# Performance work log

Hardware: AMD Instinct MI355X
Metric: run time of the kernel (lower is better)

Reference implementation:

```python
import jax, jax.numpy as jnp
import numpy as np

EPS = 1e-5  # BatchNorm eps


def _conv3x3(x, w, b):
    # x: [B,C,H,W], w: [O,C,3,3], b: [O]
    y = jax.lax.conv_general_dilated(
        x, w, window_strides=(1, 1), padding=((1, 1), (1, 1)),
        dimension_numbers=("NCHW", "OIHW", "NCHW"))
    return y + b[None, :, None, None]


def _bilinear_gather(x, py, px):
    """Bilinear sample x at fractional coords (zero outside bounds).
    x: [B,C,H,W]; py, px: [B,K,H,W] -> returns [B,C,K,H,W]."""
    B, C, H, W = x.shape
    K = py.shape[1]
    x_flat = x.reshape(B, C, H * W)
    y0 = jnp.floor(py)
    x0 = jnp.floor(px)
    wy1 = py - y0
    wx1 = px - x0
    wy0 = 1.0 - wy1
    wx0 = 1.0 - wx1

    def gather(yi, xi):
        valid = (yi >= 0) & (yi <= H - 1) & (xi >= 0) & (xi <= W - 1)
        yc = jnp.clip(yi, 0, H - 1).astype(jnp.int32)
        xc = jnp.clip(xi, 0, W - 1).astype(jnp.int32)
        idx = (yc * W + xc).reshape(B, 1, K * H * W)
        g = jnp.take_along_axis(x_flat, idx, axis=2).reshape(B, C, K, H, W)
        return g * valid.astype(x.dtype)[:, None]

    val = (gather(y0, x0) * (wy0 * wx0)[:, None]
           + gather(y0, x0 + 1.0) * (wy0 * wx1)[:, None]
           + gather(y0 + 1.0, x0) * (wy1 * wx0)[:, None]
           + gather(y0 + 1.0, x0 + 1.0) * (wy1 * wx1)[:, None])
    return val


def _deform_conv_bn_relu(x, w_off, b_off, w_dcn, b_dcn, gamma, beta):
    B, Ci, H, W = x.shape
    Co = w_dcn.shape[0]
    # offset/mask branch: 27 = 9 dy | 9 dx (cat, then interpreted interleaved) | 9 mask
    om = _conv3x3(x, w_off, b_off)                       # [B,27,H,W]
    offset = jnp.concatenate([om[:, :9], om[:, 9:18]], axis=1)  # [B,18,H,W]
    mask = jax.nn.sigmoid(om[:, 18:27])                  # [B,9,H,W]
    dy = offset[:, 0::2]                                 # [B,9,H,W]
    dx = offset[:, 1::2]                                 # [B,9,H,W]
    # base sampling grid: stride 1, pad 1, dilation 1, 3x3 kernel
    ky = jnp.repeat(jnp.arange(3, dtype=x.dtype), 3)     # [9]
    kx = jnp.tile(jnp.arange(3, dtype=x.dtype), 3)       # [9]
    hh = jnp.arange(H, dtype=x.dtype)
    ww = jnp.arange(W, dtype=x.dtype)
    py = dy + (hh - 1.0)[None, None, :, None] + ky[None, :, None, None]
    px = dx + (ww - 1.0)[None, None, None, :] + kx[None, :, None, None]
    sampled = _bilinear_gather(x, py, px)                # [B,Ci,9,H,W]
    sampled = sampled * mask[:, None]                    # modulated (DCNv2)
    out = jnp.einsum('bckhw,ock->bohw', sampled, w_dcn.reshape(Co, Ci, 9))
    out = out + b_dcn[None, :, None, None]
    # BatchNorm2d (training mode: batch statistics, biased variance) + ReLU
    mean = jnp.mean(out, axis=(0, 2, 3), keepdims=True)
    var = jnp.mean(jnp.square(out - mean), axis=(0, 2, 3), keepdims=True)
    bn = (out - mean) * jax.lax.rsqrt(var + EPS)
    bn = bn * gamma[None, :, None, None] + beta[None, :, None, None]
    return jax.nn.relu(bn)


def setup_inputs() -> dict:
    key = jax.random.key(0)
    k0, k1, k2 = jax.random.split(key, 3)
    B, Ci, Co, H, W = 2, 256, 256, 96, 96
    x = jax.random.normal(k0, (B, Ci, H, W), jnp.float32)
    # small offset-conv weights -> offsets within a few pixels (realistic after training)
    w_off = jax.random.normal(k1, (27, Ci, 3, 3), jnp.float32) * 0.01
    b_off = jnp.zeros((27,), jnp.float32)
    w_dcn = jax.random.normal(k2, (Co, Ci, 3, 3), jnp.float32) * (1.0 / np.sqrt(Ci * 9))
    b_dcn = jnp.zeros((Co,), jnp.float32)
    gamma = jnp.ones((Co,), jnp.float32)
    beta = jnp.zeros((Co,), jnp.float32)
    return {"x": x, "w_off": w_off, "b_off": b_off, "w_dcn": w_dcn,
            "b_dcn": b_dcn, "gamma": gamma, "beta": beta}


def reference(x, w_off, b_off, w_dcn, b_dcn, gamma, beta):
    return _deform_conv_bn_relu(x, w_off, b_off, w_dcn, b_dcn, gamma, beta)
```

## Files before the change

### kernel.cpp

```cpp
#include <hip/hip_runtime.h>


typedef unsigned short ushort_t;
typedef unsigned int uint_t;
typedef __attribute__((ext_vector_type(8))) short bf16x8;
typedef __attribute__((ext_vector_type(4))) float f32x4;
typedef __attribute__((ext_vector_type(2))) float f32x2v;

#define HH 96
#define WW 96
#define HWSZ 9216
#define CI 256
#define CO 256
#define NB 2
#define NPIX 18432
#define KTOT 2304

__device__ __forceinline__ uint_t f2bf(float f) {
  unsigned int u = __float_as_uint(f);
  u += 0x7fffu + ((u >> 16) & 1u);
  return u >> 16;
}
__device__ __forceinline__ float u2f(uint_t u) { return __uint_as_float(u); }
__device__ __forceinline__ float bflo(uint_t u) { return __uint_as_float(u << 16); }
__device__ __forceinline__ float bfhi(uint_t u) { return __uint_as_float(u & 0xffff0000u); }

__device__ __forceinline__ void gload16(const void* g, void* l) {
  __builtin_amdgcn_global_load_lds(
      (const __attribute__((address_space(1))) unsigned int*)g,
      (__attribute__((address_space(3))) unsigned int*)l, 16, 0, 0);
}

__global__ void cvt_w9(const float* __restrict__ w, ushort_t* __restrict__ o) {
  int i = blockIdx.x * 256 + threadIdx.x;
  int oo = i / KTOT;
  int kk = i - oo * KTOT;
  o[(kk >> 3) * 2048 + oo * 8 + (kk & 7)] = (ushort_t)f2bf(w[i]);
}

__global__ void cvt_woff9(const float* __restrict__ w, ushort_t* __restrict__ o) {
  int i = blockIdx.x * 256 + threadIdx.x;
  int m = i / KTOT;
  int kk = i - m * KTOT;
  float v = (m < 27) ? w[m * KTOT + kk] : 0.f;
  o[(kk >> 3) * 256 + m * 8 + (kk & 7)] = (ushort_t)f2bf(v);
}

__global__ __launch_bounds__(512, 2) void off_gemm(
    const float* __restrict__ x, const ushort_t* __restrict__ w27r,
    float* __restrict__ om_part) {
  __shared__ __align__(16) ushort_t A27[2][2048];
  __shared__ __align__(16) ushort_t B64[4096];
  __shared__ uint2 tbl[9][64];

  const int tid = threadIdx.x;
  const int lane = tid & 63, wid = tid >> 6;
  const int p0 = blockIdx.x * 64;
  const int part = blockIdx.y;
  const int bimg = p0 / HWSZ;
  const int hw0 = p0 - bimg * HWSZ;
  const float* xb = x + (size_t)bimg * CI * HWSZ;

  for (int e = tid; e < 576; e += 512) {
    int k = e >> 6, px = e & 63;
    int hw = hw0 + px, h = hw / WW, w_ = hw - h * WW;
    int dy = k / 3 - 1, dx = k % 3 - 1;
    bool ok = (h + dy >= 0) && (h + dy < HH) && (w_ + dx >= 0) && (w_ + dx < WW);
    tbl[k][px] = make_uint2(ok ? (uint_t)(hw + dy * WW + dx) : 0u,
                            ok ? 0x3f800000u : 0u);
  }

  const int lg = lane >> 4, lm = lane & 15;
  const int wr = wid >> 2, wc = wid & 3;
  f32x4 acc = (f32x4){0.f, 0.f, 0.f, 0.f};

  int cj[8], kj[8];
#pragma unroll
  for (int j = 0; j < 8; ++j) {
    int kk = part * 1152 + wid * 8 + j;
    cj[j] = kk / 9;
    kj[j] = kk - 9 * cj[j];
  }
  __syncthreads();

  float rv0[8], rm0[8], rv1[8], rm1[8];
  const int k0 = part * 18;

#define OG_RAW(RV, RM)                                                        \
  { _Pragma("unroll") for (int j = 0; j < 8; ++j) {                           \
      uint2 e_ = tbl[kj[j]][lane];                                            \
      RV[j] = xb[cj[j] * HWSZ + (int)e_.x];                                   \
      RM[j] = u2f(e_.y);                                                      \
      kj[j] += 1; cj[j] += 7;                                                 \
      if (kj[j] == 9) { kj[j] = 0; cj[j] += 1; } } }
#define OG_GA(CH, BUF)                                                        \
  gload16(w27r + (size_t)(CH) * 2048 + (tid & 255) * 8, &A27[BUF][(wid & 3) * 512]);
#define OG_STEP(CUR, RVC, RMC, RVN, RMN, KO)                                  \
  {                                                                           \
    if ((KO) < 17) {                                                          \
      OG_RAW(RVN, RMN)                                                        \
      OG_GA(k0 + (KO) + 1, (CUR) ^ 1)                                         \
      asm volatile("s_waitcnt vmcnt(10)" ::: "memory");                       \
    } else {                                                                  \
      asm volatile("s_waitcnt vmcnt(1)" ::: "memory");                        \
    }                                                                         \
    __builtin_amdgcn_sched_barrier(0);                                        \
    {                                                                         \
      ushort_t sv_[8] __attribute__((aligned(16)));                           \
      _Pragma("unroll") for (int j = 0; j < 8; ++j)                           \
        sv_[j] = (ushort_t)f2bf(RVC[j] * RMC[j]);                             \
      *(uint4*)&B64[tid * 8] = *(const uint4*)sv_;                            \
    }                                                                         \
    if ((KO) < 17) asm volatile("s_waitcnt vmcnt(9) lgkmcnt(0)" ::: "memory"); \
    else           asm volatile("s_waitcnt vmcnt(0) lgkmcnt(0)" ::: "memory"); \
    __builtin_amdgcn_s_barrier();                                             \
    __builtin_amdgcn_sched_barrier(0);                                        \
    _Pragma("unroll") for (int s = 0; s < 2; ++s) {                           \
      bf16x8 af = *(const bf16x8*)&A27[CUR][((s * 4 + lg) * 32 + wr * 16 + lm) * 8]; \
      bf16x8 bfv = *(const bf16x8*)&B64[((s * 4 + lg) * 64 + wc * 16 + lm) * 8];     \
      acc = __builtin_amdgcn_mfma_f32_16x16x32_bf16(af, bfv, acc, 0, 0, 0);   \
    }                                                                         \
    asm volatile("s_waitcnt lgkmcnt(0)" ::: "memory");                        \
    __builtin_amdgcn_s_barrier();                                             \
    __builtin_amdgcn_sched_barrier(0);                                        \
  }

  OG_RAW(rv0, rm0)
  OG_GA(k0, 0)
  for (int ko2 = 0; ko2 < 9; ++ko2) {
    const int ko = ko2 * 2;
    OG_STEP(0, rv0, rm0, rv1, rm1, ko)
    OG_STEP(1, rv1, rm1, rv0, rm0, ko + 1)
  }
#undef OG_RAW
#undef OG_GA
#undef OG_STEP

  int row = wr * 16 + lg * 4;
  int col = p0 + wc * 16 + lm;
#pragma unroll
  for (int r = 0; r < 4; ++r)
    if (row + r < 27)
      om_part[((size_t)(part * 27 + row + r)) * NPIX + col] = acc[r];
}

__global__ void prep_kernel(const float* __restrict__ om_part, const float* __restrict__ b_off,
                            uint_t* __restrict__ offs, float4* __restrict__ wts) {
  int n = blockIdx.x * 128 + threadIdx.x;
  float omv[27];
#pragma unroll
  for (int ch = 0; ch < 27; ++ch)
    omv[ch] = b_off[ch] + om_part[(size_t)ch * NPIX + n] +
              om_part[((size_t)(27 + ch)) * NPIX + n];
  int hw = n % HWSZ;
  int h = hw / WW, w = hw - h * WW;
#pragma unroll
  for (int k = 0; k < 9; ++k) {
    float dy = omv[2 * k], dx = omv[2 * k + 1];
    float mk = 1.f / (1.f + __expf(-omv[18 + k]));
    float py = dy + (float)(h - 1 + k / 3);
    float px = dx + (float)(w - 1 + k % 3);
    float y0f = floorf(py), x0f = floorf(px);
    int y0 = (int)y0f, x0 = (int)x0f;
    float wy1 = py - y0f, wx1 = px - x0f;
    float wy0 = 1.f - wy1, wx0 = 1.f - wx1;
    float vy0 = (y0 >= 0 && y0 <= HH - 1) ? 1.f : 0.f;
    float vy1 = (y0 + 1 >= 0 && y0 + 1 <= HH - 1) ? 1.f : 0.f;
    int yc0 = min(max(y0, 0), HH - 1), yc1 = min(max(y0 + 1, 0), HH - 1);
    int xa = min(max(x0, 0), WW - 2);
    float a_, b_;
    if (x0 >= 0 && x0 <= WW - 2)      { a_ = wx0; b_ = wx1; }
    else if (x0 == -1)                { a_ = wx1; b_ = 0.f; }
    else if (x0 == WW - 1)            { a_ = 0.f; b_ = wx0; }
    else                              { a_ = 0.f; b_ = 0.f; }
    float s0 = mk * vy0 * wy0, s1 = mk * vy1 * wy1;
    offs[(size_t)k * NPIX + n] = (uint_t)(yc0 * WW + xa) | ((uint_t)(yc1 * WW + xa) << 16);
    wts[(size_t)k * NPIX + n] = make_float4(a_ * s0, b_ * s0, a_ * s1, b_ * s1);
  }
}

__global__ __launch_bounds__(512, 1) void sample8(
    const float* __restrict__ x, const uint_t* __restrict__ offs,
    const float4* __restrict__ wts, ushort_t* __restrict__ S_g) {
  __shared__ __align__(16) uint_t xqA[HWSZ * 2];
  __shared__ __align__(16) uint_t xqB[HWSZ * 2];
  const int tid = threadIdx.x;
  const int img = blockIdx.x >> 2;
  const int quarter = blockIdx.x & 3;
  const int by = blockIdx.y;
  const int n0 = img * HWSZ + quarter * 2304;
  const int c8 = by * 8;

  {
    const float* s0 = x + ((size_t)(img * CI + c8)) * HWSZ;
#pragma unroll
    for (int i = 0; i < 9; ++i) {
      int col = i * 1024 + tid * 2;
      f32x2v c0 = *(const f32x2v*)(s0 + 0 * HWSZ + col);
      f32x2v c1 = *(const f32x2v*)(s0 + 1 * HWSZ + col);
      f32x2v c2 = *(const f32x2v*)(s0 + 2 * HWSZ + col);
      f32x2v c3 = *(const f32x2v*)(s0 + 3 * HWSZ + col);
      uint4 pkA;
      pkA.x = f2bf(c0[0]) | (f2bf(c1[0]) << 16);
      pkA.y = f2bf(c2[0]) | (f2bf(c3[0]) << 16);
      pkA.z = f2bf(c0[1]) | (f2bf(c1[1]) << 16);
      pkA.w = f2bf(c2[1]) | (f2bf(c3[1]) << 16);
      *(uint4*)&xqA[col * 2] = pkA;
      f32x2v c4 = *(const f32x2v*)(s0 + 4 * HWSZ + col);
      f32x2v c5 = *(const f32x2v*)(s0 + 5 * HWSZ + col);
      f32x2v c6 = *(const f32x2v*)(s0 + 6 * HWSZ + col);
      f32x2v c7 = *(const f32x2v*)(s0 + 7 * HWSZ + col);
      uint4 pkB;
      pkB.x = f2bf(c4[0]) | (f2bf(c5[0]) << 16);
      pkB.y = f2bf(c6[0]) | (f2bf(c7[0]) << 16);
      pkB.z = f2bf(c4[1]) | (f2bf(c5[1]) << 16);
      pkB.w = f2bf(c6[1]) | (f2bf(c7[1]) << 16);
      *(uint4*)&xqB[col * 2] = pkB;
    }
  }
  __syncthreads();

  for (int it = 0; it < 5; ++it) {
    if (it == 4 && tid >= 256) break;
    const int n = n0 + it * 512 + tid;
    uint_t ofr[9]; float4 wtr[9];
#pragma unroll
    for (int k = 0; k < 9; ++k) {
      ofr[k] = offs[(size_t)k * NPIX + n];
      wtr[k] = wts[(size_t)k * NPIX + n];
    }
    uint_t pkw[36];
#pragma unroll
    for (int i = 0; i < 36; ++i) pkw[i] = 0u;
#pragma unroll
    for (int k = 0; k < 9; ++k) {
      const int o0 = (int)(ofr[k] & 0xffffu);
      const int o1 = (int)(ofr[k] >> 16);
      const float4 wv = wtr[k];
      uint2 A00 = *(const uint2*)&xqA[o0 * 2];
      uint2 A01 = *(const uint2*)&xqA[o0 * 2 + 2];
      uint2 A10 = *(const uint2*)&xqA[o1 * 2];
      uint2 A11 = *(const uint2*)&xqA[o1 * 2 + 2];
      uint2 B00 = *(const uint2*)&xqB[o0 * 2];
      uint2 B01 = *(const uint2*)&xqB[o0 * 2 + 2];
      uint2 B10 = *(const uint2*)&xqB[o1 * 2];
      uint2 B11 = *(const uint2*)&xqB[o1 * 2 + 2];
      float v[8];
      v[0] = wv.x * bflo(A00.x) + wv.y * bflo(A01.x) + wv.z * bflo(A10.x) + wv.w * bflo(A11.x);
      v[1] = wv.x * bfhi(A00.x) + wv.y * bfhi(A01.x) + wv.z * bfhi(A10.x) + wv.w * bfhi(A11.x);
      v[2] = wv.x * bflo(A00.y) + wv.y * bflo(A01.y) + wv.z * bflo(A10.y) + wv.w * bflo(A11.y);
      v[3] = wv.x * bfhi(A00.y) + wv.y * bfhi(A01.y) + wv.z * bfhi(A10.y) + wv.w * bfhi(A11.y);
      v[4] = wv.x * bflo(B00.x) + wv.y * bflo(B01.x) + wv.z * bflo(B10.x) + wv.w * bflo(B11.x);
      v[5] = wv.x * bfhi(B00.x) + wv.y * bfhi(B01.x) + wv.z * bfhi(B10.x) + wv.w * bfhi(B11.x);
      v[6] = wv.x * bflo(B00.y) + wv.y * bflo(B01.y) + wv.z * bflo(B10.y) + wv.w * bflo(B11.y);
      v[7] = wv.x * bfhi(B00.y) + wv.y * bfhi(B01.y) + wv.z * bfhi(B10.y) + wv.w * bfhi(B11.y);
#pragma unroll
      for (int c = 0; c < 8; ++c) {
        const int q = c * 9 + k;
        pkw[q >> 1] |= f2bf(v[c]) << ((q & 1) * 16);
      }
    }
#pragma unroll
    for (int g = 0; g < 9; ++g) {
      uint4 st = make_uint4(pkw[4 * g], pkw[4 * g + 1], pkw[4 * g + 2], pkw[4 * g + 3]);
      *(uint4*)&S_g[((size_t)(9 * by + g) * NPIX + n) * 8] = st;
    }
  }
}

__global__ __launch_bounds__(512, 2) void s_gemm(
    const ushort_t* __restrict__ w9r, const ushort_t* __restrict__ S_g,
    const float* __restrict__ b_dcn, float* __restrict__ out,
    float2* __restrict__ bnp2) {
  __shared__ __align__(16) ushort_t A[4][4096];
  __shared__ __align__(16) ushort_t S[4][4096];

  const int tid = threadIdx.x;
  const int lane = tid & 63, wid = tid >> 6;
  const int p0 = blockIdx.x * 128;
  const int m0 = blockIdx.y * 128;
  const int bimg = p0 / HWSZ;
  const int hw0 = p0 - bimg * HWSZ;
  const int lg = lane >> 4, lm = lane & 15;
  const int wr = wid >> 1, wc = wid & 1;
  const int sg = tid >> 7, sp = tid & 127;

  f32x4 acc[2][4];
#pragma unroll
  for (int i = 0; i < 2; ++i)
#pragma unroll
    for (int j = 0; j < 4; ++j) acc[i][j] = (f32x4){0.f, 0.f, 0.f, 0.f};

#define SG_STAGE(CH, BUF)                                                     \
  {                                                                           \
    gload16(w9r + ((size_t)((CH) * 4 + sg) * 256 + m0 + sp) * 8,              \
            &A[BUF][(sg * 128 + sp) * 8]);                                    \
    gload16(S_g + ((size_t)((CH) * 4 + sg) * NPIX + p0 + sp) * 8,             \
            &S[BUF][(sg * 128 + sp) * 8]);                                    \
  }
#define SG_MFMA(BUF)                                                         \
  {                                                                          \
    bf16x8 af0 = *(const bf16x8*)&A[BUF][(lg * 128 + wr * 32 + lm) * 8];     \
    bf16x8 af1 = *(const bf16x8*)&A[BUF][(lg * 128 + wr * 32 + 16 + lm) * 8];\
    _Pragma("unroll") for (int ni = 0; ni < 4; ++ni) {                       \
      bf16x8 bfv = *(const bf16x8*)&S[BUF][(lg * 128 + wc * 64 + ni * 16 + lm) * 8]; \
      acc[0][ni] = __builtin_amdgcn_mfma_f32_16x16x32_bf16(af0, bfv, acc[0][ni], 0, 0, 0); \
      acc[1][ni] = __builtin_amdgcn_mfma_f32_16x16x32_bf16(af1, bfv, acc[1][ni], 0, 0, 0); \
    }                                                                        \
  }

  SG_STAGE(0, 0)
  SG_STAGE(1, 1)
  for (int ko = 0; ko < 72; ++ko) {
    if (ko < 70) {
      SG_STAGE(ko + 2, (ko + 2) & 3)
      asm volatile("s_waitcnt vmcnt(4)" ::: "memory");
    } else if (ko == 70) {
      asm volatile("s_waitcnt vmcnt(2)" ::: "memory");
    } else {
      asm volatile("s_waitcnt vmcnt(0)" ::: "memory");
    }
    __builtin_amdgcn_s_barrier();
    __builtin_amdgcn_sched_barrier(0);
    SG_MFMA(ko & 3)
  }
#undef SG_STAGE
#undef SG_MFMA

  float bsum[8], bsq[8];
#pragma unroll
  for (int mi = 0; mi < 2; ++mi) {
#pragma unroll
    for (int r = 0; r < 4; ++r) {
      int o = m0 + wr * 32 + mi * 16 + lg * 4 + r;
      float b = b_dcn[o];
      float s = 0.f, q = 0.f;
#pragma unroll
      for (int ni = 0; ni < 4; ++ni) {
        float v = acc[mi][ni][r] + b;
        out[((size_t)(bimg * CO + o)) * HWSZ + hw0 + wc * 64 + ni * 16 + lm] = v;
        s += v; q += v * v;
      }
      bsum[mi * 4 + r] = s;
      bsq[mi * 4 + r] = q;
    }
  }
#pragma unroll
  for (int d = 1; d < 16; d <<= 1) {
#pragma unroll
    for (int i = 0; i < 8; ++i) {
      bsum[i] += __shfl_xor(bsum[i], d);
      bsq[i] += __shfl_xor(bsq[i], d);
    }
  }
  asm volatile("s_waitcnt lgkmcnt(0)" ::: "memory");
  __builtin_amdgcn_s_barrier();
  float* red = (float*)&A[0][0];
  if (lm == 0) {
#pragma unroll
    for (int i = 0; i < 8; ++i) {
      int ol = wr * 32 + (i >> 2) * 16 + lg * 4 + (i & 3);
      red[ol * 2 + wc] = bsum[i];
      red[256 + ol * 2 + wc] = bsq[i];
    }
  }
  __syncthreads();
  if (tid < 128) {
    float s = red[tid * 2] + red[tid * 2 + 1];
    float q = red[256 + tid * 2] + red[256 + tid * 2 + 1];
    bnp2[(size_t)(m0 + tid) * 144 + blockIdx.x] = make_float2(s, q);
  }
}

__global__ __launch_bounds__(64) void bn_finl(const float2* __restrict__ bnp2,
                                              const float* __restrict__ gamma,
                                              const float* __restrict__ beta,
                                              float* __restrict__ ss) {
  int o = blockIdx.x, t = threadIdx.x;
  float s = 0.f, q = 0.f;
  for (int j = t; j < 144; j += 64) {
    float2 p = bnp2[(size_t)o * 144 + j];
    s += p.x; q += p.y;
  }
#pragma unroll
  for (int d = 32; d > 0; d >>= 1) {
    s += __shfl_xor(s, d);
    q += __shfl_xor(q, d);
  }
  if (t == 0) {
    float mean = s * (1.f / (float)NPIX);
    float var = q * (1.f / (float)NPIX) - mean * mean;
    float rstd = rsqrtf(var + 1e-5f);
    float sc = rstd * gamma[o];
    ss[o] = sc;
    ss[CO + o] = beta[o] - mean * sc;
  }
}

__global__ void bn_apply(float* __restrict__ out, const float* __restrict__ ss) {
  int i = blockIdx.x * 256 + threadIdx.x;
  float4 v = ((float4*)out)[i];
  int o = (i / (HWSZ / 4)) & 255;
  float sc = ss[o], sh = ss[CO + o];
  v.x = fmaxf(v.x * sc + sh, 0.f);
  v.y = fmaxf(v.y * sc + sh, 0.f);
  v.z = fmaxf(v.z * sc + sh, 0.f);
  v.w = fmaxf(v.w * sc + sh, 0.f);
  ((float4*)out)[i] = v;
}

extern "C" void kernel_launch(void* const* d_in, const int* in_sizes, int n_in,
                              void* d_out, int out_size, void* d_ws, size_t ws_size,
                              hipStream_t stream) {
  const float* x = (const float*)d_in[0];
  const float* w_off = (const float*)d_in[1];
  const float* b_off = (const float*)d_in[2];
  const float* w_dcn = (const float*)d_in[3];
  const float* b_dcn = (const float*)d_in[4];
  const float* gamma = (const float*)d_in[5];
  const float* beta = (const float*)d_in[6];
  float* out = (float*)d_out;

  char* ws = (char*)d_ws;

  size_t base = 84934656;
  ushort_t* S_g   = (ushort_t*)(ws);
  float*    om    = (float*)(ws + base);
  float2*   bnp2  = (float2*)(ws + base);
  uint_t*   offs  = (uint_t*)(ws + base + 3981312);
  float4*   wts   = (float4*)(ws + base + 4644864);
  ushort_t* w9r   = (ushort_t*)(ws + base + 7299072);
  ushort_t* w27r  = (ushort_t*)(ws + base + 8478720);
  float*    ss    = (float*)(ws + base + 8626176);

  cvt_w9<<<(CO * KTOT) / 256, 256, 0, stream>>>(w_dcn, w9r);
  cvt_woff9<<<(32 * KTOT) / 256, 256, 0, stream>>>(w_off, w27r);
  off_gemm<<<dim3(NPIX / 64, 2), 512, 0, stream>>>(x, w27r, om);
  prep_kernel<<<NPIX / 128, 128, 0, stream>>>(om, b_off, offs, wts);
  sample8<<<dim3(8, 32), 512, 0, stream>>>(x, offs, wts, S_g);
  s_gemm<<<dim3(NPIX / 128, 2), 512, 0, stream>>>(w9r, S_g, b_dcn, out, bnp2);
  bn_finl<<<CO, 64, 0, stream>>>(bnp2, gamma, beta, ss);
  bn_apply<<<(out_size / 4) / 256, 256, 0, stream>>>(out, ss);
}
```

Baseline: 132.4 us.

## Load GEMM fragments directly from global memory into registers, bypassing LDS staging

The s_gemm kernel no longer stages A and S tiles through a 4-deep LDS ring with barriers. Each wave now loads its own bf16x8 MFMA fragments straight from global memory into registers, double-buffered in two register sets. This removes the LDS round trip and the per-iteration block barrier. In exchange, fragments shared by waves are fetched redundantly from global/L2, since A is reused across the 2 column waves and S across the 4 row waves, which raises cache traffic. Latency hiding now relies on only two chunks of register prefetch.

```diff
diff --git a/kernel.cpp b/kernel.cpp
--- a/kernel.cpp
+++ b/kernel.cpp
@@ -272,8 +272,7 @@
     const ushort_t* __restrict__ w9r, const ushort_t* __restrict__ S_g,
     const float* __restrict__ b_dcn, float* __restrict__ out,
     float2* __restrict__ bnp2) {
-  __shared__ __align__(16) ushort_t A[4][4096];
-  __shared__ __align__(16) ushort_t S[4][4096];
+  __shared__ float red[512];
 
   const int tid = threadIdx.x;
   const int lane = tid & 63, wid = tid >> 6;
@@ -283,7 +282,10 @@
   const int hw0 = p0 - bimg * HWSZ;
   const int lg = lane >> 4, lm = lane & 15;
   const int wr = wid >> 1, wc = wid & 1;
-  const int sg = tid >> 7, sp = tid & 127;
+
+  const ushort_t* pa = w9r + ((size_t)lg * 256 + m0 + wr * 32 + lm) * 8;
+  const ushort_t* ps = S_g + ((size_t)lg * NPIX + p0 + wc * 64 + lm) * 8;
+  const size_t SSTR = (size_t)4 * NPIX * 8;
 
   f32x4 acc[2][4];
 #pragma unroll
@@ -291,41 +293,47 @@
 #pragma unroll
     for (int j = 0; j < 4; ++j) acc[i][j] = (f32x4){0.f, 0.f, 0.f, 0.f};
 
-#define SG_STAGE(CH, BUF)                                                     \
+#define SG_LOAD(CH, A0_, A1_, B0_, B1_, B2_, B3_)                             \
   {                                                                           \
-    gload16(w9r + ((size_t)((CH) * 4 + sg) * 256 + m0 + sp) * 8,              \
-            &A[BUF][(sg * 128 + sp) * 8]);                                    \
-    gload16(S_g + ((size_t)((CH) * 4 + sg) * NPIX + p0 + sp) * 8,             \
-            &S[BUF][(sg * 128 + sp) * 8]);                                    \
-  }
-#define SG_MFMA(BUF)                                                         \
-  {                                                                          \
-    bf16x8 af0 = *(const bf16x8*)&A[BUF][(lg * 128 + wr * 32 + lm) * 8];     \
-    bf16x8 af1 = *(const bf16x8*)&A[BUF][(lg * 128 + wr * 32 + 16 + lm) * 8];\
-    _Pragma("unroll") for (int ni = 0; ni < 4; ++ni) {                       \
-      bf16x8 bfv = *(const bf16x8*)&S[BUF][(lg * 128 + wc * 64 + ni * 16 + lm) * 8]; \
-      acc[0][ni] = __builtin_amdgcn_mfma_f32_16x16x32_bf16(af0, bfv, acc[0][ni], 0, 0, 0); \
-      acc[1][ni] = __builtin_amdgcn_mfma_f32_16x16x32_bf16(af1, bfv, acc[1][ni], 0, 0, 0); \
-    }                                                                        \
-  }
-
-  SG_STAGE(0, 0)
-  SG_STAGE(1, 1)
-  for (int ko = 0; ko < 72; ++ko) {
-    if (ko < 70) {
-      SG_STAGE(ko + 2, (ko + 2) & 3)
-      asm volatile("s_waitcnt vmcnt(4)" ::: "memory");
-    } else if (ko == 70) {
-      asm volatile("s_waitcnt vmcnt(2)" ::: "memory");
-    } else {
-      asm volatile("s_waitcnt vmcnt(0)" ::: "memory");
-    }
-    __builtin_amdgcn_s_barrier();
-    __builtin_amdgcn_sched_barrier(0);
-    SG_MFMA(ko & 3)
-  }
-#undef SG_STAGE
-#undef SG_MFMA
+    const ushort_t* pa_ = pa + (size_t)(CH) * 8192;                           \
+    A0_ = *(const bf16x8*)(pa_);                                              \
+    A1_ = *(const bf16x8*)(pa_ + 128);                                        \
+    const ushort_t* ps_ = ps + (size_t)(CH) * SSTR;                           \
+    B0_ = *(const bf16x8*)(ps_);                                              \
+    B1_ = *(const bf16x8*)(ps_ + 128);                                        \
+    B2_ = *(const bf16x8*)(ps_ + 256);                                        \
+    B3_ = *(const bf16x8*)(ps_ + 384);                                        \
+  }
+#define SG_MM(A0_, A1_, B0_, B1_, B2_, B3_)                                   \
+  {                                                                           \
+    acc[0][0] = __builtin_amdgcn_mfma_f32_16x16x32_bf16(A0_, B0_, acc[0][0], 0, 0, 0); \
+    acc[1][0] = __builtin_amdgcn_mfma_f32_16x16x32_bf16(A1_, B0_, acc[1][0], 0, 0, 0); \
+    acc[0][1] = __builtin_amdgcn_mfma_f32_16x16x32_bf16(A0_, B1_, acc[0][1], 0, 0, 0); \
+    acc[1][1] = __builtin_amdgcn_mfma_f32_16x16x32_bf16(A1_, B1_, acc[1][1], 0, 0, 0); \
+    acc[0][2] = __builtin_amdgcn_mfma_f32_16x16x32_bf16(A0_, B2_, acc[0][2], 0, 0, 0); \
+    acc[1][2] = __builtin_amdgcn_mfma_f32_16x16x32_bf16(A1_, B2_, acc[1][2], 0, 0, 0); \
+    acc[0][3] = __builtin_amdgcn_mfma_f32_16x16x32_bf16(A0_, B3_, acc[0][3], 0, 0, 0); \
+    acc[1][3] = __builtin_amdgcn_mfma_f32_16x16x32_bf16(A1_, B3_, acc[1][3], 0, 0, 0); \
+  }
+
+  bf16x8 xa0, xa1, xb0, xb1, xb2, xb3;
+  bf16x8 ya0, ya1, yb0, yb1, yb2, yb3;
+  SG_LOAD(0, xa0, xa1, xb0, xb1, xb2, xb3)
+  SG_LOAD(1, ya0, ya1, yb0, yb1, yb2, yb3)
+  for (int ko = 0; ko < 68; ko += 2) {
+    SG_MM(xa0, xa1, xb0, xb1, xb2, xb3)
+    SG_LOAD(ko + 2, xa0, xa1, xb0, xb1, xb2, xb3)
+    SG_MM(ya0, ya1, yb0, yb1, yb2, yb3)
+    SG_LOAD(ko + 3, ya0, ya1, yb0, yb1, yb2, yb3)
+  }
+  SG_MM(xa0, xa1, xb0, xb1, xb2, xb3)
+  SG_LOAD(70, xa0, xa1, xb0, xb1, xb2, xb3)
+  SG_MM(ya0, ya1, yb0, yb1, yb2, yb3)
+  SG_LOAD(71, ya0, ya1, yb0, yb1, yb2, yb3)
+  SG_MM(xa0, xa1, xb0, xb1, xb2, xb3)
+  SG_MM(ya0, ya1, yb0, yb1, yb2, yb3)
+#undef SG_LOAD
+#undef SG_MM
 
   float bsum[8], bsq[8];
 #pragma unroll
@@ -353,9 +361,6 @@
       bsq[i] += __shfl_xor(bsq[i], d);
     }
   }
-  asm volatile("s_waitcnt lgkmcnt(0)" ::: "memory");
-  __builtin_amdgcn_s_barrier();
-  float* red = (float*)&A[0][0];
   if (lm == 0) {
 #pragma unroll
     for (int i = 0; i < 8; ++i) {
```

Measured after the change: 155.5 us. +17.4%, slower.
